# Performance work log

Hardware: AMD Instinct MI355X
Metric: run time of the kernel (lower is better)

The kernel has to match this reference:

```python
import jax, jax.numpy as jnp
import numpy as np

N_NODES = 50000
N_EDGES = 800000
F_IN = 64
CHANNELS = 64
ATTN_SLOPE = 0.2   # GATConv internal LeakyReLU on attention logits
OUT_SLOPE = 0.3    # wrapper's LeakyReLU(alpha=0.3)


def setup_inputs() -> dict:
    key = jax.random.key(0)
    ks = jax.random.split(key, 7)
    x = jax.random.normal(ks[0], (N_NODES, F_IN), dtype=jnp.float32)
    edge_src = jax.random.randint(ks[1], (N_EDGES,), 0, N_NODES, dtype=jnp.int64)
    edge_dst = jax.random.randint(ks[2], (N_EDGES,), 0, N_NODES, dtype=jnp.int64)
    # Learned parameters (single attention head)
    W = jax.random.normal(ks[3], (F_IN, CHANNELS), dtype=jnp.float32) / np.sqrt(F_IN)
    a_src = jax.random.normal(ks[4], (CHANNELS,), dtype=jnp.float32) / np.sqrt(CHANNELS)
    a_dst = jax.random.normal(ks[5], (CHANNELS,), dtype=jnp.float32) / np.sqrt(CHANNELS)
    b = jnp.zeros((CHANNELS,), dtype=jnp.float32)
    return {"x": x, "W": W, "a_src": a_src, "a_dst": a_dst, "b": b,
            "edge_src": edge_src, "edge_dst": edge_dst}


def reference(x, W, a_src, a_dst, b, edge_src, edge_dst):
    N = x.shape[0]
    h = x @ W                                  # [N, C] transformed features
    s_src = h @ a_src                          # [N] per-node source score
    s_dst = h @ a_dst                          # [N] per-node dest score
    # Per-edge attention logits, LeakyReLU(0.2) as in GAT
    e = jax.nn.leaky_relu(s_src[edge_src] + s_dst[edge_dst], ATTN_SLOPE)  # [E]
    # Numerically stable softmax over each destination's neighborhood
    m = jax.ops.segment_max(e, edge_dst, num_segments=N)                  # [N]
    ex = jnp.exp(e - m[edge_dst])                                         # [E]
    denom = jax.ops.segment_sum(ex, edge_dst, num_segments=N)             # [N]
    alpha = ex / jnp.maximum(denom[edge_dst], 1e-9)                       # [E]
    # Scatter-aggregate weighted neighbor features
    out = jax.ops.segment_sum(alpha[:, None] * h[edge_src], edge_dst,
                              num_segments=N) + b                         # [N, C]
    return jax.nn.leaky_relu(out, OUT_SLOPE)
```

## Files before the change

### kernel.cpp

```cpp
#include <hip/hip_runtime.h>
#include <hip/hip_fp16.h>

#define N_NODES 50000
#define N_EDGES 800000
#define CH 64
#define FT_NODES 32
#define FT_BLKS ((N_NODES + FT_NODES - 1) / FT_NODES)
#define NB 782
#define NCHK 784
#define ECHUNK ((N_EDGES + NCHK - 1) / NCHK)
#define LCAP 2048

static constexpr size_t alignup16(size_t x) { return (x + 15) & ~(size_t)15; }
static const size_t OFF_H      = 0;
static const size_t OFF_SSRC   = alignup16(OFF_H      + (size_t)N_NODES*CH*2);
static const size_t OFF_SDST   = alignup16(OFF_SSRC   + (size_t)N_NODES*4);
static const size_t OFF_HIST   = alignup16(OFF_SDST   + (size_t)N_NODES*4);
static const size_t OFF_BTOT   = alignup16(OFF_HIST   + (size_t)NCHK*NB*4);
static const size_t OFF_CB     = alignup16(OFF_BTOT   + (size_t)NB*4);
static const size_t OFF_ROWPTR = alignup16(OFF_CB     + (size_t)(NB+1)*4);
static const size_t OFF_BUCK   = alignup16(OFF_ROWPTR + (size_t)(N_NODES+4)*4);
static const size_t OFF_SPERM  = alignup16(OFF_BUCK   + (size_t)N_EDGES*4);

__global__ __launch_bounds__(256) void k_feat(
        const float* __restrict__ x, const float* __restrict__ W,
        const float* __restrict__ a_src, const float* __restrict__ a_dst,
        const int* __restrict__ edst,
        __half* __restrict__ h, float* __restrict__ ssrc, float* __restrict__ sdst,
        unsigned int* __restrict__ hist) {
    __shared__ float Ws[64 * 64];
    __shared__ float xs[FT_NODES][68];
    __shared__ unsigned int lh[NB];
    const int tid = threadIdx.x;
    const bool do_hist = (blockIdx.x < NCHK);
    if (do_hist)
        for (int j = tid; j < NB; j += 256) lh[j] = 0u;
#pragma unroll
    for (int i = 0; i < 16; ++i) Ws[tid + i * 256] = W[tid + i * 256];
    const int n0 = blockIdx.x * FT_NODES;
    const int nvalid = min(FT_NODES, N_NODES - n0);
    const float4* x4 = (const float4*)(x + (size_t)n0 * CH);
    for (int i = tid; i < nvalid * 16; i += 256) {
        const int n = i >> 4, q = i & 15;
        *(float4*)&xs[n][q * 4] = x4[i];
    }
    __syncthreads();
    if (do_hist) {
        const int st = blockIdx.x * ECHUNK;
        const int en = min(st + ECHUNK, N_EDGES);
        for (int i = st + tid; i < en; i += 256)
            atomicAdd(&lh[((unsigned int)edst[i]) >> 6], 1u);
    }
    const int nl = tid >> 3;
    const int g = tid & 7;
    const int c0 = g * 8;
    const int node = n0 + nl;
    if (nl < nvalid) {
        float acc[8] = {0.f, 0.f, 0.f, 0.f, 0.f, 0.f, 0.f, 0.f};
#pragma unroll
        for (int k = 0; k < 64; ++k) {
            const float xv = xs[nl][k];
            const float4 w0 = *(const float4*)&Ws[k * 64 + c0];
            const float4 w1 = *(const float4*)&Ws[k * 64 + c0 + 4];
            acc[0] = fmaf(xv, w0.x, acc[0]);
            acc[1] = fmaf(xv, w0.y, acc[1]);
            acc[2] = fmaf(xv, w0.z, acc[2]);
            acc[3] = fmaf(xv, w0.w, acc[3]);
            acc[4] = fmaf(xv, w1.x, acc[4]);
            acc[5] = fmaf(xv, w1.y, acc[5]);
            acc[6] = fmaf(xv, w1.z, acc[6]);
            acc[7] = fmaf(xv, w1.w, acc[7]);
        }
        __half2 hv[4];
#pragma unroll
        for (int i = 0; i < 4; ++i) hv[i] = __floats2half2_rn(acc[2 * i], acc[2 * i + 1]);
        *(float4*)(h + (size_t)node * CH + c0) = *(float4*)hv;
        float ps = 0.f, pd = 0.f;
#pragma unroll
        for (int i = 0; i < 8; ++i) {
            ps = fmaf(acc[i], a_src[c0 + i], ps);
            pd = fmaf(acc[i], a_dst[c0 + i], pd);
        }
#pragma unroll
        for (int off = 4; off; off >>= 1) {
            ps += __shfl_xor(ps, off);
            pd += __shfl_xor(pd, off);
        }
        if (g == 0) { ssrc[node] = ps; sdst[node] = pd; }
    }
    if (do_hist) {
        __syncthreads();
        for (int j = tid; j < NB; j += 256)
            hist[(size_t)blockIdx.x * NB + j] = lh[j];
    }
}

__global__ __launch_bounds__(256) void k_bintot(
        const unsigned int* __restrict__ hist, unsigned int* __restrict__ bintot) {
    __shared__ unsigned int red[256];
    const int t = threadIdx.x, b = blockIdx.x;
    unsigned int v = 0u;
    for (int c = t; c < NCHK; c += 256) v += hist[(size_t)c * NB + b];
    red[t] = v;
    __syncthreads();
#pragma unroll
    for (int off = 128; off; off >>= 1) {
        if (t < off) red[t] += red[t + off];
        __syncthreads();
    }
    if (t == 0) bintot[b] = red[0];
}

__global__ __launch_bounds__(256) void k_rewrite(
        const unsigned int* __restrict__ bintot, unsigned int* __restrict__ hist,
        unsigned int* __restrict__ cb) {
    __shared__ unsigned int lcol[NCHK];
    __shared__ unsigned int red[256];
    __shared__ unsigned int sc[256];
    const int t = threadIdx.x, b = blockIdx.x;
    unsigned int v = 0u;
    for (int j = t; j < b; j += 256) v += bintot[j];
    red[t] = v;
    for (int c = t; c < NCHK; c += 256) lcol[c] = hist[(size_t)c * NB + b];
    __syncthreads();
#pragma unroll
    for (int off = 128; off; off >>= 1) {
        if (t < off) red[t] += red[t + off];
        __syncthreads();
    }
    const unsigned int cbb = red[0];
    if (t == 0) { cb[b] = cbb; if (b == NB - 1) cb[NB] = N_EDGES; }
    unsigned int part = 0u;
    const int c0 = 4 * t;
    if (t < 196) {
#pragma unroll
        for (int q = 0; q < 4; ++q) part += lcol[c0 + q];
    }
    sc[t] = part;
    __syncthreads();
#pragma unroll
    for (int off = 1; off < 256; off <<= 1) {
        unsigned int u = (t >= off) ? sc[t - off] : 0u;
        __syncthreads();
        sc[t] += u;
        __syncthreads();
    }
    if (t < 196) {
        unsigned int run = cbb + sc[t] - part;
#pragma unroll
        for (int q = 0; q < 4; ++q) {
            const unsigned int tmp = lcol[c0 + q];
            lcol[c0 + q] = run;
            run += tmp;
        }
    }
    __syncthreads();
    for (int c = t; c < NCHK; c += 256) hist[(size_t)c * NB + b] = lcol[c];
}

__global__ __launch_bounds__(256) void k_scatter(
        const int* __restrict__ esrc, const int* __restrict__ edst,
        const unsigned int* __restrict__ hist, unsigned int* __restrict__ buck) {
    __shared__ unsigned int wp[NB];
    const int t = threadIdx.x, blk = blockIdx.x;
    for (int j = t; j < NB; j += 256) wp[j] = hist[(size_t)blk * NB + j];
    __syncthreads();
    const int st = blk * ECHUNK;
    const int en = min(st + ECHUNK, N_EDGES);
    for (int i = st + t; i < en; i += 256) {
        const unsigned int d = (unsigned int)edst[i];
        const unsigned int pos = atomicAdd(&wp[d >> 6], 1u);
        buck[pos] = (d << 16) | (unsigned int)esrc[i];
    }
}

__global__ __launch_bounds__(256) void k_csr(
        const unsigned int* __restrict__ buck, const unsigned int* __restrict__ cb,
        int* __restrict__ row_ptr, unsigned short* __restrict__ src_perm) {
    __shared__ unsigned int cnt[64];
    __shared__ unsigned int wp[64];
    __shared__ unsigned short lsrc[LCAP];
    const int t = threadIdx.x, blk = blockIdx.x;
    const int start = (int)cb[blk];
    const int end = (int)cb[blk + 1];
    const int m = end - start;
    if (t < 64) cnt[t] = 0u;
    __syncthreads();
    for (int i = start + t; i < end; i += 256)
        atomicAdd(&cnt[(buck[i] >> 16) & 63u], 1u);
    __syncthreads();
    if (t < 64) {
        const unsigned int own = cnt[t];
        unsigned int incl = own;
#pragma unroll
        for (int d = 1; d < 64; d <<= 1) {
            const unsigned int v = __shfl_up(incl, d);
            if (t >= d) incl += v;
        }
        const unsigned int excl = incl - own;
        wp[t] = excl;
        const int node = blk * 64 + t;
        if (node <= N_NODES) row_ptr[node] = start + (int)excl;
    }
    __syncthreads();
    if (m <= LCAP) {
        for (int i = start + t; i < end; i += 256) {
            const unsigned int rec = buck[i];
            const unsigned int pos = atomicAdd(&wp[(rec >> 16) & 63u], 1u);
            lsrc[pos] = (unsigned short)(rec & 0xFFFFu);
        }
        __syncthreads();
        for (int p = t; p < m; p += 256)
            src_perm[start + p] = lsrc[p];
    } else {
        for (int i = start + t; i < end; i += 256) {
            const unsigned int rec = buck[i];
            const unsigned int pos = atomicAdd(&wp[(rec >> 16) & 63u], 1u);
            src_perm[start + (int)pos] = (unsigned short)(rec & 0xFFFFu);
        }
    }
}

__global__ __launch_bounds__(256) void k_node_agg(
        const unsigned short* __restrict__ src_perm, const int* __restrict__ row_ptr,
        const float* __restrict__ ssrc, const float* __restrict__ sdst,
        const __half* __restrict__ h, const float* __restrict__ b,
        float* __restrict__ out) {
    const int tid = threadIdx.x;
    const int lane = tid & 63;
    const int node = blockIdx.x * 4 + (tid >> 6);
    const int row = row_ptr[node];
    const int deg = row_ptr[node + 1] - row;
    const float sd = sdst[node];
    const int slot = lane >> 4;
    const int c4 = lane & 15;
    float4 acc = make_float4(0.f, 0.f, 0.f, 0.f);
    float wsum = 0.f;
    for (int base = 0; base < deg; base += 64) {
        const int j = base + lane;
        int s = 0;
        float w = 0.f;
        if (j < deg) {
            s = (int)src_perm[row + j];
            float e = ssrc[s] + sd;
            e = (e > 0.f) ? e : 0.2f * e;
            w = __expf(e);
        }
        wsum += w;
        const int cnt_t = min(64, deg - base);
        for (int j2 = 0; j2 < cnt_t; j2 += 16) {
            float a[4]; int si[4]; float2 raw[4];
#pragma unroll
            for (int q = 0; q < 4; ++q) {
                const int e = j2 + 4 * q + slot;
                a[q] = __shfl(w, e);
                si[q] = __shfl(s, e);
            }
#pragma unroll
            for (int q = 0; q < 4; ++q)
                raw[q] = *(const float2*)&h[(size_t)si[q] * CH + 4 * c4];
#pragma unroll
            for (int q = 0; q < 4; ++q) {
                union { float2 f2; __half2 h2[2]; } u;
                u.f2 = raw[q];
                const float2 lo = __half22float2(u.h2[0]);
                const float2 hi = __half22float2(u.h2[1]);
                acc.x = fmaf(a[q], lo.x, acc.x);
                acc.y = fmaf(a[q], lo.y, acc.y);
                acc.z = fmaf(a[q], hi.x, acc.z);
                acc.w = fmaf(a[q], hi.y, acc.w);
            }
        }
    }
    acc.x += __shfl_xor(acc.x, 16); acc.x += __shfl_xor(acc.x, 32);
    acc.y += __shfl_xor(acc.y, 16); acc.y += __shfl_xor(acc.y, 32);
    acc.z += __shfl_xor(acc.z, 16); acc.z += __shfl_xor(acc.z, 32);
    acc.w += __shfl_xor(acc.w, 16); acc.w += __shfl_xor(acc.w, 32);
#pragma unroll
    for (int off = 32; off; off >>= 1) wsum += __shfl_xor(wsum, off);
    if (lane < 16) {
        const float inv = 1.f / fmaxf(wsum, 1e-9f);
        const float4 bb = *(const float4*)&b[4 * c4];
        float vx = acc.x * inv + bb.x;
        float vy = acc.y * inv + bb.y;
        float vz = acc.z * inv + bb.z;
        float vw = acc.w * inv + bb.w;
        vx = (vx > 0.f) ? vx : 0.3f * vx;
        vy = (vy > 0.f) ? vy : 0.3f * vy;
        vz = (vz > 0.f) ? vz : 0.3f * vz;
        vw = (vw > 0.f) ? vw : 0.3f * vw;
        *(float4*)&out[(size_t)node * CH + 4 * c4] = make_float4(vx, vy, vz, vw);
    }
}

extern "C" void kernel_launch(void* const* d_in, const int* in_sizes, int n_in,
                              void* d_out, int out_size, void* d_ws, size_t ws_size,
                              hipStream_t stream) {
    const float* x     = (const float*)d_in[0];
    const float* W     = (const float*)d_in[1];
    const float* a_src = (const float*)d_in[2];
    const float* a_dst = (const float*)d_in[3];
    const float* b     = (const float*)d_in[4];
    const int* esrc    = (const int*)d_in[5];
    const int* edst    = (const int*)d_in[6];
    float* out = (float*)d_out;

    char* ws = (char*)d_ws;
    __half* h                = (__half*)(ws + OFF_H);
    float* ssrc              = (float*)(ws + OFF_SSRC);
    float* sdst              = (float*)(ws + OFF_SDST);
    unsigned int* hist       = (unsigned int*)(ws + OFF_HIST);
    unsigned int* bintot     = (unsigned int*)(ws + OFF_BTOT);
    unsigned int* cb         = (unsigned int*)(ws + OFF_CB);
    int* row_ptr             = (int*)(ws + OFF_ROWPTR);
    unsigned int* buck       = (unsigned int*)(ws + OFF_BUCK);
    unsigned short* src_perm = (unsigned short*)(ws + OFF_SPERM);

    k_feat<<<FT_BLKS, 256, 0, stream>>>(x, W, a_src, a_dst, edst, h, ssrc, sdst, hist);
    k_bintot<<<NB, 256, 0, stream>>>(hist, bintot);
    k_rewrite<<<NB, 256, 0, stream>>>(bintot, hist, cb);
    k_scatter<<<NCHK, 256, 0, stream>>>(esrc, edst, hist, buck);
    k_csr<<<NB, 256, 0, stream>>>(buck, cb, row_ptr, src_perm);
    k_node_agg<<<N_NODES / 4, 256, 0, stream>>>(src_perm, row_ptr, ssrc, sdst, h, b, out);
}
```

Measured before the change: 77.83 us.

## Process two nodes per thread in feature GEMM and two nodes per wave in aggregation

The feature kernel now computes two nodes per thread (64 nodes per block), reusing each W load across both. This halves the block count and aligns it with the 782 histogram chunks, so the do_hist branch is removed. The aggregation kernel maps two destination nodes to each 64-lane wave, 32 lanes per node, so low-degree nodes leave fewer lanes idle, and it issues eight gathers per inner step. The cost is loop divergence up to the larger degree of the paired nodes, plus more registers per thread in both kernels.

```diff
diff --git a/kernel.cpp b/kernel.cpp
--- a/kernel.cpp
+++ b/kernel.cpp
@@ -4,10 +4,10 @@
 #define N_NODES 50000
 #define N_EDGES 800000
 #define CH 64
-#define FT_NODES 32
+#define FT_NODES 64
 #define FT_BLKS ((N_NODES + FT_NODES - 1) / FT_NODES)
 #define NB 782
-#define NCHK 784
+#define NCHK 782
 #define ECHUNK ((N_EDGES + NCHK - 1) / NCHK)
 #define LCAP 2048
 
@@ -32,9 +32,7 @@
     __shared__ float xs[FT_NODES][68];
     __shared__ unsigned int lh[NB];
     const int tid = threadIdx.x;
-    const bool do_hist = (blockIdx.x < NCHK);
-    if (do_hist)
-        for (int j = tid; j < NB; j += 256) lh[j] = 0u;
+    for (int j = tid; j < NB; j += 256) lh[j] = 0u;
 #pragma unroll
     for (int i = 0; i < 16; ++i) Ws[tid + i * 256] = W[tid + i * 256];
     const int n0 = blockIdx.x * FT_NODES;
@@ -45,7 +43,7 @@
         *(float4*)&xs[n][q * 4] = x4[i];
     }
     __syncthreads();
-    if (do_hist) {
+    {
         const int st = blockIdx.x * ECHUNK;
         const int en = min(st + ECHUNK, N_EDGES);
         for (int i = st + tid; i < en; i += 256)
@@ -54,45 +52,55 @@
     const int nl = tid >> 3;
     const int g = tid & 7;
     const int c0 = g * 8;
-    const int node = n0 + nl;
-    if (nl < nvalid) {
-        float acc[8] = {0.f, 0.f, 0.f, 0.f, 0.f, 0.f, 0.f, 0.f};
-#pragma unroll
-        for (int k = 0; k < 64; ++k) {
-            const float xv = xs[nl][k];
-            const float4 w0 = *(const float4*)&Ws[k * 64 + c0];
-            const float4 w1 = *(const float4*)&Ws[k * 64 + c0 + 4];
-            acc[0] = fmaf(xv, w0.x, acc[0]);
-            acc[1] = fmaf(xv, w0.y, acc[1]);
-            acc[2] = fmaf(xv, w0.z, acc[2]);
-            acc[3] = fmaf(xv, w0.w, acc[3]);
-            acc[4] = fmaf(xv, w1.x, acc[4]);
-            acc[5] = fmaf(xv, w1.y, acc[5]);
-            acc[6] = fmaf(xv, w1.z, acc[6]);
-            acc[7] = fmaf(xv, w1.w, acc[7]);
-        }
+    const int nodeA = n0 + 2 * nl;
+    const bool vA = (2 * nl < nvalid);
+    const bool vB = (2 * nl + 1 < nvalid);
+    float accA[8] = {0,0,0,0,0,0,0,0};
+    float accB[8] = {0,0,0,0,0,0,0,0};
+#pragma unroll
+    for (int k = 0; k < 64; ++k) {
+        const float xv0 = xs[2 * nl][k];
+        const float xv1 = xs[2 * nl + 1][k];
+        const float4 w0 = *(const float4*)&Ws[k * 64 + c0];
+        const float4 w1 = *(const float4*)&Ws[k * 64 + c0 + 4];
+        accA[0] = fmaf(xv0, w0.x, accA[0]); accB[0] = fmaf(xv1, w0.x, accB[0]);
+        accA[1] = fmaf(xv0, w0.y, accA[1]); accB[1] = fmaf(xv1, w0.y, accB[1]);
+        accA[2] = fmaf(xv0, w0.z, accA[2]); accB[2] = fmaf(xv1, w0.z, accB[2]);
+        accA[3] = fmaf(xv0, w0.w, accA[3]); accB[3] = fmaf(xv1, w0.w, accB[3]);
+        accA[4] = fmaf(xv0, w1.x, accA[4]); accB[4] = fmaf(xv1, w1.x, accB[4]);
+        accA[5] = fmaf(xv0, w1.y, accA[5]); accB[5] = fmaf(xv1, w1.y, accB[5]);
+        accA[6] = fmaf(xv0, w1.z, accA[6]); accB[6] = fmaf(xv1, w1.z, accB[6]);
+        accA[7] = fmaf(xv0, w1.w, accA[7]); accB[7] = fmaf(xv1, w1.w, accB[7]);
+    }
+    float psA = 0.f, pdA = 0.f, psB = 0.f, pdB = 0.f;
+#pragma unroll
+    for (int i = 0; i < 8; ++i) {
+        const float as = a_src[c0 + i], ad = a_dst[c0 + i];
+        psA = fmaf(accA[i], as, psA); pdA = fmaf(accA[i], ad, pdA);
+        psB = fmaf(accB[i], as, psB); pdB = fmaf(accB[i], ad, pdB);
+    }
+#pragma unroll
+    for (int off = 4; off; off >>= 1) {
+        psA += __shfl_xor(psA, off); pdA += __shfl_xor(pdA, off);
+        psB += __shfl_xor(psB, off); pdB += __shfl_xor(pdB, off);
+    }
+    if (vA) {
         __half2 hv[4];
 #pragma unroll
-        for (int i = 0; i < 4; ++i) hv[i] = __floats2half2_rn(acc[2 * i], acc[2 * i + 1]);
-        *(float4*)(h + (size_t)node * CH + c0) = *(float4*)hv;
-        float ps = 0.f, pd = 0.f;
-#pragma unroll
-        for (int i = 0; i < 8; ++i) {
-            ps = fmaf(acc[i], a_src[c0 + i], ps);
-            pd = fmaf(acc[i], a_dst[c0 + i], pd);
-        }
-#pragma unroll
-        for (int off = 4; off; off >>= 1) {
-            ps += __shfl_xor(ps, off);
-            pd += __shfl_xor(pd, off);
-        }
-        if (g == 0) { ssrc[node] = ps; sdst[node] = pd; }
-    }
-    if (do_hist) {
-        __syncthreads();
-        for (int j = tid; j < NB; j += 256)
-            hist[(size_t)blockIdx.x * NB + j] = lh[j];
-    }
+        for (int i = 0; i < 4; ++i) hv[i] = __floats2half2_rn(accA[2 * i], accA[2 * i + 1]);
+        *(float4*)(h + (size_t)nodeA * CH + c0) = *(float4*)hv;
+        if (g == 0) { ssrc[nodeA] = psA; sdst[nodeA] = pdA; }
+    }
+    if (vB) {
+        __half2 hv[4];
+#pragma unroll
+        for (int i = 0; i < 4; ++i) hv[i] = __floats2half2_rn(accB[2 * i], accB[2 * i + 1]);
+        *(float4*)(h + (size_t)(nodeA + 1) * CH + c0) = *(float4*)hv;
+        if (g == 0) { ssrc[nodeA + 1] = psB; sdst[nodeA + 1] = pdB; }
+    }
+    __syncthreads();
+    for (int j = tid; j < NB; j += 256)
+        hist[(size_t)blockIdx.x * NB + j] = lh[j];
 }
 
 __global__ __launch_bounds__(256) void k_bintot(
@@ -114,14 +122,14 @@
 __global__ __launch_bounds__(256) void k_rewrite(
         const unsigned int* __restrict__ bintot, unsigned int* __restrict__ hist,
         unsigned int* __restrict__ cb) {
-    __shared__ unsigned int lcol[NCHK];
+    __shared__ unsigned int lcol[784];
     __shared__ unsigned int red[256];
     __shared__ unsigned int sc[256];
     const int t = threadIdx.x, b = blockIdx.x;
     unsigned int v = 0u;
     for (int j = t; j < b; j += 256) v += bintot[j];
     red[t] = v;
-    for (int c = t; c < NCHK; c += 256) lcol[c] = hist[(size_t)c * NB + b];
+    for (int c = t; c < 784; c += 256) lcol[c] = (c < NCHK) ? hist[(size_t)c * NB + b] : 0u;
     __syncthreads();
 #pragma unroll
     for (int off = 128; off; off >>= 1) {
@@ -228,16 +236,20 @@
         float* __restrict__ out) {
     const int tid = threadIdx.x;
     const int lane = tid & 63;
-    const int node = blockIdx.x * 4 + (tid >> 6);
+    const int wid = tid >> 6;
+    const int half = lane >> 5;
+    const int hl = lane & 31;
+    const int slot = hl >> 4;
+    const int c4 = hl & 15;
+    const int node = blockIdx.x * 8 + wid * 2 + half;
     const int row = row_ptr[node];
     const int deg = row_ptr[node + 1] - row;
     const float sd = sdst[node];
-    const int slot = lane >> 4;
-    const int c4 = lane & 15;
+    const int degmax = max(deg, __shfl_xor(deg, 32));
     float4 acc = make_float4(0.f, 0.f, 0.f, 0.f);
     float wsum = 0.f;
-    for (int base = 0; base < deg; base += 64) {
-        const int j = base + lane;
+    for (int base = 0; base < degmax; base += 32) {
+        const int j = base + hl;
         int s = 0;
         float w = 0.f;
         if (j < deg) {
@@ -247,20 +259,20 @@
             w = __expf(e);
         }
         wsum += w;
-        const int cnt_t = min(64, deg - base);
+        const int cnt_t = min(32, degmax - base);
         for (int j2 = 0; j2 < cnt_t; j2 += 16) {
-            float a[4]; int si[4]; float2 raw[4];
-#pragma unroll
-            for (int q = 0; q < 4; ++q) {
-                const int e = j2 + 4 * q + slot;
-                a[q] = __shfl(w, e);
-                si[q] = __shfl(s, e);
+            float a[8]; int si[8]; float2 raw[8];
+#pragma unroll
+            for (int q = 0; q < 8; ++q) {
+                const int srcl = half * 32 + j2 + 2 * q + slot;
+                a[q] = __shfl(w, srcl);
+                si[q] = __shfl(s, srcl);
             }
 #pragma unroll
-            for (int q = 0; q < 4; ++q)
+            for (int q = 0; q < 8; ++q)
                 raw[q] = *(const float2*)&h[(size_t)si[q] * CH + 4 * c4];
 #pragma unroll
-            for (int q = 0; q < 4; ++q) {
+            for (int q = 0; q < 8; ++q) {
                 union { float2 f2; __half2 h2[2]; } u;
                 u.f2 = raw[q];
                 const float2 lo = __half22float2(u.h2[0]);
@@ -272,13 +284,13 @@
             }
         }
     }
-    acc.x += __shfl_xor(acc.x, 16); acc.x += __shfl_xor(acc.x, 32);
-    acc.y += __shfl_xor(acc.y, 16); acc.y += __shfl_xor(acc.y, 32);
-    acc.z += __shfl_xor(acc.z, 16); acc.z += __shfl_xor(acc.z, 32);
-    acc.w += __shfl_xor(acc.w, 16); acc.w += __shfl_xor(acc.w, 32);
-#pragma unroll
-    for (int off = 32; off; off >>= 1) wsum += __shfl_xor(wsum, off);
-    if (lane < 16) {
+    acc.x += __shfl_xor(acc.x, 16);
+    acc.y += __shfl_xor(acc.y, 16);
+    acc.z += __shfl_xor(acc.z, 16);
+    acc.w += __shfl_xor(acc.w, 16);
+#pragma unroll
+    for (int off = 16; off; off >>= 1) wsum += __shfl_xor(wsum, off);
+    if (hl < 16) {
         const float inv = 1.f / fmaxf(wsum, 1e-9f);
         const float4 bb = *(const float4*)&b[4 * c4];
         float vx = acc.x * inv + bb.x;
@@ -321,5 +333,5 @@
     k_rewrite<<<NB, 256, 0, stream>>>(bintot, hist, cb);
     k_scatter<<<NCHK, 256, 0, stream>>>(esrc, edst, hist, buck);
     k_csr<<<NB, 256, 0, stream>>>(buck, cb, row_ptr, src_perm);
-    k_node_agg<<<N_NODES / 4, 256, 0, stream>>>(src_perm, row_ptr, ssrc, sdst, h, b, out);
-}
+    k_node_agg<<<N_NODES / 8, 256, 0, stream>>>(src_perm, row_ptr, ssrc, sdst, h, b, out);
+}
```

Result: faster. 73.53 us (-5.5%).
